# Performance work log

Hardware: AMD Instinct MI355X
Metric: run time of the kernel (lower is better)

Reference implementation:

```python
import jax, jax.numpy as jnp
import numpy as np

T, F, C, V, H, E, S = 256, 32, 8, 10000, 1024, 256, 512
PAD, BOS, EOS = 0, 1, 2


def setup_inputs() -> dict:
    key = jax.random.key(0)
    ks = jax.random.split(key, 16)
    sH = 1.0 / np.sqrt(H).astype(np.float32)
    inp = {
        'token_ctx': jax.random.normal(ks[0], (1, S, H), jnp.float32),
        'char_emb_w': jax.random.normal(ks[1], (V, E), jnp.float32) * 0.02,
        'enc_W_ih': jax.random.normal(ks[2], (3 * H, E), jnp.float32) * sH,
        'enc_W_hh': jax.random.normal(ks[3], (3 * H, H), jnp.float32) * sH,
        'enc_b_ih': jnp.zeros((3 * H,), jnp.float32),
        'enc_b_hh': jnp.zeros((3 * H,), jnp.float32),
        'dec_W_ih': jax.random.normal(ks[4], (3 * H, E), jnp.float32) * sH,
        'dec_W_hh': jax.random.normal(ks[5], (3 * H, H), jnp.float32) * sH,
        'dec_b_ih': jnp.zeros((3 * H,), jnp.float32),
        'dec_b_hh': jnp.zeros((3 * H,), jnp.float32),
        'out_W': jax.random.normal(ks[6], (V, H), jnp.float32) * sH,
        'out_b': jnp.zeros((V,), jnp.float32),
    }
    # (token_id, xtoken_idx, char_id) triples; every token 1..T has exactly C chars
    tok_ids = jnp.repeat(jnp.arange(1, T + 1, dtype=jnp.int32), C)
    xt_ids = jax.random.randint(ks[7], (T * C,), 0, S, jnp.int32)
    ch_ids = jax.random.randint(ks[8], (T * C,), 4, V, jnp.int32)  # avoid specials
    inp['in_sent_token_chars'] = jnp.stack([tok_ids, xt_ids, ch_ids], axis=-1)[None]
    gold = jax.random.randint(ks[9], (T * F,), 4, V, jnp.int32)  # no EOS -> full-length decode
    inp['out_chars'] = jnp.concatenate([jnp.array([BOS], jnp.int32), gold])[None]
    inp['max_tokens'] = T
    inp['max_form_len'] = F
    inp['use_teacher_forcing'] = 1
    return inp


def _gru_cell(x, h, W_ih, W_hh, b_ih, b_hh):
    # PyTorch GRU cell convention; x:[T,E], h:[T,H]
    gi = x @ W_ih.T + b_ih
    gh = h @ W_hh.T + b_hh
    i_r, i_z, i_n = jnp.split(gi, 3, axis=-1)
    h_r, h_z, h_n = jnp.split(gh, 3, axis=-1)
    r = jax.nn.sigmoid(i_r + h_r)
    z = jax.nn.sigmoid(i_z + h_z)
    n = jnp.tanh(i_n + r * h_n)
    return (1.0 - z) * n + z * h


def reference(token_ctx, char_emb_w, enc_W_ih, enc_W_hh, enc_b_ih, enc_b_hh,
              dec_W_ih, dec_W_hh, dec_b_ih, dec_b_hh, out_W, out_b,
              in_sent_token_chars, out_chars, max_tokens, max_form_len,
              use_teacher_forcing):
    Vout = out_b.shape[0]
    # ragged mask select per token id -> here every token has exactly C chars
    tc = in_sent_token_chars[0].reshape(max_tokens, -1, 3)  # [T, C, 3]
    chars = tc[:, :, 2]          # [T, C]
    xtoken_ids = tc[:, :, 1]     # [T, C]
    # enc_state = mean over the token's xtoken contexts
    h0 = jnp.mean(token_ctx[0][xtoken_ids], axis=1)  # [T, H]
    # ---- encoder GRU over the token's chars (batched over tokens) ----
    x_enc = char_emb_w[chars]  # [T, C, E]

    def enc_step(h, x):
        return _gru_cell(x, h, enc_W_ih, enc_W_hh, enc_b_ih, enc_b_hh), None

    h_enc, _ = jax.lax.scan(enc_step, h0, jnp.swapaxes(x_enc, 0, 1))  # [T, H]
    # ---- decoder GRU, max_form_len steps, teacher-forced, EOS freeze+pad ----
    # gold char for token t at step s is out_chars[0, t*F + s + 1]
    gold = out_chars[0, 1:1 + max_tokens * max_form_len].reshape(max_tokens, max_form_len)
    c0 = jnp.full((max_tokens,), out_chars[0, 0], dtype=out_chars.dtype)
    done0 = (c0 == EOS)
    last0 = jnp.zeros((max_tokens, Vout), jnp.float32)

    def dec_step(carry, g):
        h, c, done, last = carry
        x = char_emb_w[c]
        h_new = _gru_cell(x, h, dec_W_ih, dec_W_hh, dec_b_ih, dec_b_hh)
        s_new = h_new @ out_W.T + out_b
        score = jnp.where(done[:, None], last, s_new)  # pad with last score after EOS
        h = jnp.where(done[:, None], h, h_new)         # state frozen after EOS
        if use_teacher_forcing:
            c_next = g
        else:
            c_next = jnp.argmax(s_new, axis=-1).astype(c.dtype)
        done = done | (c_next == EOS)
        return (h, c_next, done, score), score

    _, scores = jax.lax.scan(dec_step, (h_enc, c0, done0, last0),
                             jnp.swapaxes(gold, 0, 1))  # [F, T, V]
    # torch.cat(dec_scores, dim=1): token-major, step-minor -> [1, T*F, V]
    return jnp.transpose(scores, (1, 0, 2)).reshape(1, max_tokens * max_form_len, Vout)
```

## Files before the change

### kernel.cpp

```cpp
#include <hip/hip_runtime.h>
#include <hip/hip_bf16.h>
#include <math.h>

#define TT   256
#define FF   32
#define CCH  8
#define VV   10000
#define HH   1024
#define EE   256
#define NG   3072
#define EOS_ID 2
#define NSTEPS 40
#define CHAIN_BLKS 256
#define CTR_INTS 512

typedef __attribute__((ext_vector_type(8))) short bf16x8;
typedef __attribute__((ext_vector_type(4))) float f32x4;

__device__ __forceinline__ void gload_lds16(const void* g, void* l) {
    __builtin_amdgcn_global_load_lds((const __attribute__((address_space(1))) void*)g,
                                     (__attribute__((address_space(3))) void*)l,
                                     16, 0, 0);
}

__device__ __forceinline__ float sigmf(float x) { return 1.f / (1.f + __expf(-x)); }

__global__ __launch_bounds__(256) void prep_kernel(const int* __restrict__ oc,
                                                   int* __restrict__ c_in,
                                                   unsigned char* __restrict__ done,
                                                   int* __restrict__ ctr) {
    int t = threadIdx.x;
    for (int i = t; i < CTR_INTS; i += 256) ctr[i] = 0;
    int c0 = oc[0];
    bool d = (c0 == EOS_ID);
    for (int f = 0; f < FF; ++f) {
        c_in[t * FF + f] = (f == 0) ? c0 : oc[1 + t * FF + f - 1];
        done[t * FF + f] = d ? 1 : 0;
        d = d || (oc[1 + t * FF + f] == EOS_ID);
    }
}

__global__ __launch_bounds__(256) void h0_kernel(const float* __restrict__ tctx,
                                                 const int* __restrict__ sent,
                                                 float* __restrict__ h,
                                                 __hip_bfloat16* __restrict__ A0) {
    int t = blockIdx.x;
    int tid = threadIdx.x;
    __shared__ int xt[CCH];
    if (tid < CCH) xt[tid] = sent[(t * CCH + tid) * 3 + 1];
    __syncthreads();
#pragma unroll
    for (int jj = 0; jj < 4; ++jj) {
        int j = tid + jj * 256;
        float s = 0.f;
#pragma unroll
        for (int c = 0; c < CCH; ++c) s += tctx[(size_t)xt[c] * HH + j];
        float hv = s * 0.125f;
        h[(size_t)t * HH + j] = hv;
        A0[(size_t)t * HH + j] = __float2bfloat16(hv);
    }
}

__global__ __launch_bounds__(256) void f2b_kernel(const float* __restrict__ src,
                                                  __hip_bfloat16* __restrict__ dst) {
    size_t base = ((size_t)blockIdx.x * 256 + threadIdx.x) * 4;
    float4 v = *(const float4*)(src + base);
    dst[base + 0] = __float2bfloat16(v.x);
    dst[base + 1] = __float2bfloat16(v.y);
    dst[base + 2] = __float2bfloat16(v.z);
    dst[base + 3] = __float2bfloat16(v.w);
}

__global__ __launch_bounds__(256) void build_Bg(const float* __restrict__ Whh,
                                                __hip_bfloat16* __restrict__ Bg) {
    int by = blockIdx.x;
    int tid = threadIdx.x;
    int jbrow = by & 127;
    int jb = by >> 7;
    int g = jbrow >> 5, ji = jbrow & 31;
    __hip_bfloat16* drow = Bg + (size_t)by * HH;
    if (g < 3) {
        const float* srow = Whh + (size_t)(g * 1024 + jb * 32 + ji) * HH;
        float4 v = *(const float4*)(srow + tid * 4);
        drow[tid * 4 + 0] = __float2bfloat16(v.x);
        drow[tid * 4 + 1] = __float2bfloat16(v.y);
        drow[tid * 4 + 2] = __float2bfloat16(v.z);
        drow[tid * 4 + 3] = __float2bfloat16(v.w);
    } else {
        __hip_bfloat16 z = __float2bfloat16(0.f);
        drow[tid * 4 + 0] = z; drow[tid * 4 + 1] = z;
        drow[tid * 4 + 2] = z; drow[tid * 4 + 3] = z;
    }
}

template<int MODE>
__global__ __launch_bounds__(256) void gemm_pipe(const __hip_bfloat16* __restrict__ A, int lda,
                                                 const __hip_bfloat16* __restrict__ B, int ldb,
                                                 float* __restrict__ C,
                                                 const int* __restrict__ idsrc,
                                                 int NIT) {
    __shared__ __hip_bfloat16 As[4][128 * 32];
    __shared__ __hip_bfloat16 Bs[4][128 * 32];
    __shared__ int sids[128];

    const int tid = threadIdx.x;
    const int n0 = blockIdx.x * 128;
    const int m0 = blockIdx.y * 128;

    if (tid < 128) {
        int row = m0 + tid;
        int t = row & 255;
        int id;
        if (MODE == 1) { int c = row >> 8; id = idsrc[(t * CCH + c) * 3 + 2]; }
        else           { int f = row >> 8; id = idsrc[t * FF + f]; }
        sids[tid] = id;
    }
    __syncthreads();

    const int srow = tid >> 2, skq = tid & 3;
    const int l = tid & 63;
    const int w = tid >> 6;
    const int wr = (w >> 1) * 64, wc = (w & 1) * 64;
    const int fra = ((wr + (l & 15)) << 5) + ((l >> 4) << 3);
    const int frb = ((wc + (l & 15)) << 5) + ((l >> 4) << 3);

    f32x4 acc[4][4];
#pragma unroll
    for (int i = 0; i < 4; ++i)
#pragma unroll
        for (int j = 0; j < 4; ++j) acc[i][j] = (f32x4){0.f, 0.f, 0.f, 0.f};

    auto stage = [&](int slot, int it) {
        const int k0 = it * 32;
        const __hip_bfloat16* ga0 = A + (size_t)sids[srow] * lda + k0 + skq * 8;
        const __hip_bfloat16* ga1 = A + (size_t)sids[64 + srow] * lda + k0 + skq * 8;
        const __hip_bfloat16* gb0 = B + (size_t)(n0 + srow) * ldb + k0 + skq * 8;
        const __hip_bfloat16* gb1 = B + (size_t)(n0 + 64 + srow) * ldb + k0 + skq * 8;
        __hip_bfloat16* lA = &As[slot][tid * 8];
        __hip_bfloat16* lB = &Bs[slot][tid * 8];
        gload_lds16(ga0, lA);
        gload_lds16(ga1, lA + 2048);
        gload_lds16(gb0, lB);
        gload_lds16(gb1, lB + 2048);
    };

    stage(0, 0);
    stage(1, 1);

    for (int it = 0; it < NIT; ++it) {
        if (it + 2 < NIT) stage((it + 2) & 3, it + 2);
        int ahead = NIT - 1 - it; if (ahead > 2) ahead = 2;
        if (ahead >= 2)      asm volatile("s_waitcnt vmcnt(8)" ::: "memory");
        else if (ahead == 1) asm volatile("s_waitcnt vmcnt(4)" ::: "memory");
        else                 asm volatile("s_waitcnt vmcnt(0)" ::: "memory");
        __builtin_amdgcn_s_barrier();
        __builtin_amdgcn_sched_barrier(0);

        const __hip_bfloat16* cA = As[it & 3];
        const __hip_bfloat16* cB = Bs[it & 3];
        bf16x8 af[4], bfv[4];
#pragma unroll
        for (int fm = 0; fm < 4; ++fm) af[fm] = *(const bf16x8*)&cA[fra + fm * 512];
#pragma unroll
        for (int fn = 0; fn < 4; ++fn) bfv[fn] = *(const bf16x8*)&cB[frb + fn * 512];
#pragma unroll
        for (int fm = 0; fm < 4; ++fm)
#pragma unroll
            for (int fn = 0; fn < 4; ++fn)
                acc[fm][fn] = __builtin_amdgcn_mfma_f32_16x16x32_bf16(af[fm], bfv[fn], acc[fm][fn], 0, 0, 0);
    }

    const int colb = wc + (l & 15);
    const int rb   = wr + ((l >> 4) << 2);
#pragma unroll
    for (int fm = 0; fm < 4; ++fm)
#pragma unroll
        for (int fn = 0; fn < 4; ++fn)
#pragma unroll
            for (int q = 0; q < 4; ++q)
                C[(size_t)(m0 + rb + fm * 16 + q) * NG + n0 + colb + fn * 16] = acc[fm][fn][q];
}

__global__ __launch_bounds__(256, 1) void chain_kernel(
    __hip_bfloat16* Abuf0, __hip_bfloat16* Abuf1,
    const __hip_bfloat16* __restrict__ Bg_e,
    const __hip_bfloat16* __restrict__ Bg_d,
    const float* __restrict__ gi_enc, const float* __restrict__ gi_dec,
    const float* __restrict__ ebih, const float* __restrict__ ebhh,
    const float* __restrict__ dbih, const float* __restrict__ dbhh,
    const float* __restrict__ hA,
    __hip_bfloat16* __restrict__ hsb,
    const unsigned char* __restrict__ dflags,
    int* flags) {

    __shared__ __align__(16) char smem[52224];

    const int tid = threadIdx.x;
    const int b = blockIdx.x;
    const int mt = b >> 5, jb = b & 31;
    const int m0 = mt * 32;

    const int l = tid & 63, w = tid >> 6;
    const int wr = (w >> 1) * 16;
    const int wc = (w & 1) * 48;
    const int ji = tid & 31;
    const int tr0 = tid >> 5;
    const int j = jb * 32 + ji;

    float* gp = (float*)(smem + 36864);
    __hip_bfloat16* stb = (__hip_bfloat16*)(smem + 36864 + 12800);

    float hreg[4];
#pragma unroll
    for (int p = 0; p < 4; ++p)
        hreg[p] = hA[(size_t)(m0 + p * 8 + tr0) * HH + j];

    const float e_br = ebih[j] + ebhh[j];
    const float e_bz = ebih[HH + j] + ebhh[HH + j];
    const float e_bi = ebih[2 * HH + j];
    const float e_bh = ebhh[2 * HH + j];
    const float d_br = dbih[j] + dbhh[j];
    const float d_bz = dbih[HH + j] + dbhh[HH + j];
    const float d_bi = dbih[2 * HH + j];
    const float d_bh = dbhh[2 * HH + j];

    auto stageB = [&](const __hip_bfloat16* Bp, int slot, int it) {
        char* sb = smem + slot * 12288;
#pragma unroll
        for (int c = 0; c < 3; ++c) {
            int chunk = c * 256 + tid;
            int row = chunk >> 3, q = chunk & 7;
            const __hip_bfloat16* src =
                Bp + (size_t)(jb * 128 + row) * HH + it * 64 + ((q ^ (row & 7)) << 3);
            gload_lds16(src, sb + chunk * 16);
        }
    };

    stageB(Bg_e, 0, 0);
    stageB(Bg_e, 1, 1);

    float gr[4], gz[4], gn_[4];
    int dfl[4] = {0, 0, 0, 0};
#pragma unroll
    for (int p = 0; p < 4; ++p) {
        const float* gb = gi_enc + (size_t)(m0 + p * 8 + tr0) * NG + j;
        asm volatile("global_load_dword %0, %1, off nt" : "=v"(gr[p])  : "v"(gb));
        asm volatile("global_load_dword %0, %1, off nt" : "=v"(gz[p])  : "v"(gb + HH));
        asm volatile("global_load_dword %0, %1, off nt" : "=v"(gn_[p]) : "v"(gb + 2 * HH));
    }

    for (int s = 0; s < NSTEPS; ++s) {
        const __hip_bfloat16* Ab = (s & 1) ? Abuf1 : Abuf0;
        __hip_bfloat16* An = (s & 1) ? Abuf0 : Abuf1;
        const __hip_bfloat16* Bg = (s < CCH) ? Bg_e : Bg_d;

        const __hip_bfloat16* aptr = Ab + (size_t)(m0 + wr + (l & 15)) * HH + ((l >> 4) << 3);
        bf16x8 av[16][2];
#pragma unroll
        for (int it = 0; it < 16; ++it) {
            asm volatile("global_load_dwordx4 %0, %1, off sc0 sc1"
                         : "=v"(av[it][0]) : "v"(aptr + it * 64));
            asm volatile("global_load_dwordx4 %0, %1, off sc0 sc1"
                         : "=v"(av[it][1]) : "v"(aptr + it * 64 + 32));
        }

        f32x4 acc[3];
        acc[0] = (f32x4){0.f, 0.f, 0.f, 0.f};
        acc[1] = (f32x4){0.f, 0.f, 0.f, 0.f};
        acc[2] = (f32x4){0.f, 0.f, 0.f, 0.f};

#pragma unroll
        for (int it = 0; it < 16; ++it) {
            if (it + 2 < 16) stageB(Bg, (it + 2) % 3, it + 2);
            if (it == 0)       asm volatile("s_waitcnt vmcnt(33)" ::: "memory");
            else if (it == 1)  asm volatile("s_waitcnt vmcnt(34)" ::: "memory");
            else if (it <= 13) asm volatile("s_waitcnt vmcnt(6)"  ::: "memory");
            else if (it == 14) asm volatile("s_waitcnt vmcnt(3)"  ::: "memory");
            else               asm volatile("s_waitcnt vmcnt(0)"  ::: "memory");
            __builtin_amdgcn_s_barrier();
            __builtin_amdgcn_sched_barrier(0);

            const __hip_bfloat16* cB = (const __hip_bfloat16*)(smem + (it % 3) * 12288);
#pragma unroll
            for (int kh = 0; kh < 2; ++kh) {
                const int qg = kh * 4 + (l >> 4);
                bf16x8 bf0, bf1, bf2;
                { int r_ = wc + (l & 15);      bf0 = *(const bf16x8*)&cB[r_ * 64 + ((qg ^ (r_ & 7)) << 3)]; }
                { int r_ = wc + 16 + (l & 15); bf1 = *(const bf16x8*)&cB[r_ * 64 + ((qg ^ (r_ & 7)) << 3)]; }
                { int r_ = wc + 32 + (l & 15); bf2 = *(const bf16x8*)&cB[r_ * 64 + ((qg ^ (r_ & 7)) << 3)]; }
                acc[0] = __builtin_amdgcn_mfma_f32_16x16x32_bf16(av[it][kh], bf0, acc[0], 0, 0, 0);
                acc[1] = __builtin_amdgcn_mfma_f32_16x16x32_bf16(av[it][kh], bf1, acc[1], 0, 0, 0);
                acc[2] = __builtin_amdgcn_mfma_f32_16x16x32_bf16(av[it][kh], bf2, acc[2], 0, 0, 0);
            }
        }

        {
            const int rb = wr + ((l >> 4) << 2);
#pragma unroll
            for (int fn = 0; fn < 3; ++fn)
#pragma unroll
                for (int q = 0; q < 4; ++q)
                    gp[(rb + q) * 100 + wc + fn * 16 + (l & 15)] = acc[fn][q];
        }
        __syncthreads();

        const int f = s - CCH;
        const float br_ = (s < CCH) ? e_br : d_br;
        const float bz_ = (s < CCH) ? e_bz : d_bz;
        const float bi_ = (s < CCH) ? e_bi : d_bi;
        const float bh_ = (s < CCH) ? e_bh : d_bh;
#pragma unroll
        for (int p = 0; p < 4; ++p) {
            const int tr = p * 8 + tr0;
            float racc = gp[tr * 100 + ji];
            float zacc = gp[tr * 100 + 32 + ji];
            float nacc = gp[tr * 100 + 64 + ji];
            float r = sigmf(gr[p] + br_ + racc);
            float z = sigmf(gz[p] + bz_ + zacc);
            float n = tanhf(gn_[p] + bi_ + r * (nacc + bh_));
            float hold = hreg[p];
            float hv = (1.f - z) * n + z * hold;
            if (s >= CCH && dfl[p]) hv = hold;
            hreg[p] = hv;
            stb[tr * 32 + ji] = __float2bfloat16(hv);
        }
        __syncthreads();

        if (tid < 128) {
            const int row = tid >> 2, part = tid & 3;
            bf16x8 v = *(const bf16x8*)&stb[row * 32 + part * 8];
            if (s < NSTEPS - 1) {
                const __hip_bfloat16* ap = An + (size_t)(m0 + row) * HH + jb * 32 + part * 8;
                asm volatile("global_store_dwordx4 %0, %1, off sc0 sc1"
                             :: "v"(ap), "v"(v) : "memory");
            }
            if (s >= CCH) {
                bf16x8* hp = (bf16x8*)(hsb + ((size_t)f * TT + m0 + row) * HH + jb * 32 + part * 8);
                __builtin_nontemporal_store(v, hp);
            }
        }

        if (s < NSTEPS - 1) {
            const __hip_bfloat16* BgN = (s + 1 < CCH) ? Bg_e : Bg_d;
            stageB(BgN, 0, 0);
            stageB(BgN, 1, 1);
            asm volatile("s_waitcnt vmcnt(6)" ::: "memory");
            __syncthreads();

            if (tid == 0) {
                int v = s + 1;
                int* fp = flags + (mt << 5) + jb;
                asm volatile("global_store_dword %0, %1, off sc0 sc1"
                             :: "v"(fp), "v"(v) : "memory");
            }

            {
                const float* gnext = (s + 1 < CCH) ? (gi_enc + (size_t)(s + 1) * TT * NG)
                                                   : (gi_dec + (size_t)(s + 1 - CCH) * TT * NG);
#pragma unroll
                for (int p = 0; p < 4; ++p) {
                    const float* gb = gnext + (size_t)(m0 + p * 8 + tr0) * NG + j;
                    asm volatile("global_load_dword %0, %1, off nt" : "=v"(gr[p])  : "v"(gb));
                    asm volatile("global_load_dword %0, %1, off nt" : "=v"(gz[p])  : "v"(gb + HH));
                    asm volatile("global_load_dword %0, %1, off nt" : "=v"(gn_[p]) : "v"(gb + 2 * HH));
                }
                if (s + 1 >= CCH) {
                    const int fnx = s + 1 - CCH;
#pragma unroll
                    for (int p = 0; p < 4; ++p) {
                        const unsigned char* dp = dflags + (size_t)(m0 + p * 8 + tr0) * FF + fnx;
                        asm volatile("global_load_ubyte %0, %1, off" : "=v"(dfl[p]) : "v"(dp));
                    }
                }
            }

            if (tid < 64) {
                const int* fp = flags + (mt << 5) + (tid & 31);
                const int target = s + 1;
                long guard = 0;
                for (;;) {
                    int v = target;
                    if (tid < 32) {
                        asm volatile("global_load_dword %0, %1, off sc0 sc1"
                                     : "=v"(v) : "v"(fp));
                        asm volatile("s_waitcnt vmcnt(0)" ::: "memory");
                    }
                    if (__all(v >= target)) break;
                    if (++guard > (1L << 22)) break;
                    __builtin_amdgcn_s_sleep(4);
                }
            }
            __syncthreads();
        }
    }
}

__global__ __launch_bounds__(256) void scores_pipe(const __hip_bfloat16* __restrict__ hsb,
                                                   const __hip_bfloat16* __restrict__ Wb,
                                                   const float* __restrict__ bout,
                                                   const int* __restrict__ oc,
                                                   float* __restrict__ out) {
    __shared__ __hip_bfloat16 As[4][128 * 32];
    __shared__ __hip_bfloat16 Bs[4][128 * 32];
    int bid = blockIdx.x;
    int sid = (bid & 7) * 632 + (bid >> 3);
    int bx = sid % 79, by = sid / 79;
    int n0 = bx * 128, m0 = by * 128;

    const int tid = threadIdx.x;
    const int l = tid & 63;
    const int w = tid >> 6;
    const int wr = (w >> 1) * 64, wc = (w & 1) * 64;
    const int srow = tid >> 2, skq = tid & 3;

    f32x4 acc[4][4];
#pragma unroll
    for (int i = 0; i < 4; ++i)
#pragma unroll
        for (int j = 0; j < 4; ++j) acc[i][j] = (f32x4){0.f, 0.f, 0.f, 0.f};

    int br0 = n0 + srow, br1 = n0 + 64 + srow;
    br0 = (br0 > VV - 1) ? VV - 1 : br0;
    br1 = (br1 > VV - 1) ? VV - 1 : br1;
    const __hip_bfloat16* gA0 = hsb + (size_t)(m0 + srow) * HH + skq * 8;
    const __hip_bfloat16* gA1 = hsb + (size_t)(m0 + 64 + srow) * HH + skq * 8;
    const __hip_bfloat16* gB0 = Wb + (size_t)br0 * HH + skq * 8;
    const __hip_bfloat16* gB1 = Wb + (size_t)br1 * HH + skq * 8;
    const int fra = ((wr + (l & 15)) << 5) + ((l >> 4) << 3);
    const int frb = ((wc + (l & 15)) << 5) + ((l >> 4) << 3);

    auto stage = [&](int slot, int it) {
        const int k0 = it * 32;
        __hip_bfloat16* lA = &As[slot][tid * 8];
        __hip_bfloat16* lB = &Bs[slot][tid * 8];
        gload_lds16(gA0 + k0, lA);
        gload_lds16(gA1 + k0, lA + 2048);
        gload_lds16(gB0 + k0, lB);
        gload_lds16(gB1 + k0, lB + 2048);
    };

    stage(0, 0);
    stage(1, 1);

    for (int it = 0; it < 32; ++it) {
        if (it + 2 < 32) stage((it + 2) & 3, it + 2);
        int ahead = 31 - it; if (ahead > 2) ahead = 2;
        if (ahead >= 2)      asm volatile("s_waitcnt vmcnt(8)" ::: "memory");
        else if (ahead == 1) asm volatile("s_waitcnt vmcnt(4)" ::: "memory");
        else                 asm volatile("s_waitcnt vmcnt(0)" ::: "memory");
        __builtin_amdgcn_s_barrier();
        __builtin_amdgcn_sched_barrier(0);

        const __hip_bfloat16* cA = As[it & 3];
        const __hip_bfloat16* cB = Bs[it & 3];
        bf16x8 af[4], bfv[4];
#pragma unroll
        for (int fm = 0; fm < 4; ++fm) af[fm] = *(const bf16x8*)&cA[fra + fm * 512];
#pragma unroll
        for (int fn = 0; fn < 4; ++fn) bfv[fn] = *(const bf16x8*)&cB[frb + fn * 512];
#pragma unroll
        for (int fm = 0; fm < 4; ++fm)
#pragma unroll
            for (int fn = 0; fn < 4; ++fn)
                acc[fm][fn] = __builtin_amdgcn_mfma_f32_16x16x32_bf16(af[fm], bfv[fn], acc[fm][fn], 0, 0, 0);
    }

    const bool zf = (oc[0] == EOS_ID);
    const int colb = wc + (l & 15);
    const int rb   = wr + ((l >> 4) << 2);
#pragma unroll
    for (int fn = 0; fn < 4; ++fn) {
        int v = n0 + colb + fn * 16;
        if (v < VV) {
            float bb = bout[v];
#pragma unroll
            for (int fm = 0; fm < 4; ++fm) {
#pragma unroll
                for (int q = 0; q < 4; ++q) {
                    int m = m0 + rb + fm * 16 + q;
                    int fo = m >> 8, t = m & 255;
                    float val = zf ? 0.f : (acc[fm][fn][q] + bb);
                    __builtin_nontemporal_store(val, &out[(size_t)(t * FF + fo) * VV + v]);
                }
            }
        }
    }
}

extern "C" void kernel_launch(void* const* d_in, const int* in_sizes, int n_in,
                              void* d_out, int out_size, void* d_ws, size_t ws_size,
                              hipStream_t stream) {
    (void)in_sizes; (void)n_in; (void)ws_size;

    const float* token_ctx = (const float*)d_in[0];
    const float* emb       = (const float*)d_in[1];
    const float* eWih      = (const float*)d_in[2];
    const float* eWhh      = (const float*)d_in[3];
    const float* ebih      = (const float*)d_in[4];
    const float* ebhh      = (const float*)d_in[5];
    const float* dWih      = (const float*)d_in[6];
    const float* dWhh      = (const float*)d_in[7];
    const float* dbih      = (const float*)d_in[8];
    const float* dbhh      = (const float*)d_in[9];
    const float* Wout      = (const float*)d_in[10];
    const float* bout      = (const float*)d_in[11];
    const int*   sent      = (const int*)d_in[12];
    const int*   ochars    = (const int*)d_in[13];
    float* out = (float*)d_out;

    char* w = (char*)d_ws;
    float* hA = (float*)w;                      w += (size_t)TT * HH * 4;
    __hip_bfloat16* Ab0 = (__hip_bfloat16*)w;   w += (size_t)TT * HH * 2;
    __hip_bfloat16* Ab1 = (__hip_bfloat16*)w;   w += (size_t)TT * HH * 2;
    __hip_bfloat16* hsb = (__hip_bfloat16*)w;   w += (size_t)FF * TT * HH * 2;
    __hip_bfloat16* Woutb = (__hip_bfloat16*)w; w += (size_t)VV * HH * 2;
    int* c_in = (int*)w;                        w += (size_t)TT * FF * 4;
    unsigned char* done = (unsigned char*)w;    w += (size_t)TT * FF;
    w = (char*)(((size_t)w + 255) & ~(size_t)255);
    int* ctr = (int*)w;                         w += (size_t)CTR_INTS * 4;

    char* tail = (char*)d_out + (size_t)out_size * 4;
    tail -= (size_t)32 * 128 * HH * 2;    __hip_bfloat16* Bg_e = (__hip_bfloat16*)tail;
    tail -= (size_t)32 * 128 * HH * 2;    __hip_bfloat16* Bg_d = (__hip_bfloat16*)tail;
    tail -= (size_t)CCH * TT * NG * 4;    float* gi_enc = (float*)tail;
    tail -= (size_t)FF * TT * NG * 4;     float* gi_dec = (float*)tail;
    tail -= (size_t)VV * EE * 2;          __hip_bfloat16* emb_bf = (__hip_bfloat16*)tail;
    tail -= (size_t)NG * EE * 2;          __hip_bfloat16* Wihb_e = (__hip_bfloat16*)tail;
    tail -= (size_t)NG * EE * 2;          __hip_bfloat16* Wihb_d = (__hip_bfloat16*)tail;

    prep_kernel<<<1, 256, 0, stream>>>(ochars, c_in, done, ctr);
    h0_kernel<<<TT, 256, 0, stream>>>(token_ctx, sent, hA, Ab0);
    f2b_kernel<<<(VV * EE) / 4 / 256, 256, 0, stream>>>(emb, emb_bf);
    f2b_kernel<<<(NG * EE) / 4 / 256, 256, 0, stream>>>(eWih, Wihb_e);
    f2b_kernel<<<(NG * EE) / 4 / 256, 256, 0, stream>>>(dWih, Wihb_d);
    f2b_kernel<<<(VV * HH) / 4 / 256, 256, 0, stream>>>(Wout, Woutb);
    build_Bg<<<4096, 256, 0, stream>>>(eWhh, Bg_e);
    build_Bg<<<4096, 256, 0, stream>>>(dWhh, Bg_d);

    gemm_pipe<1><<<dim3(24, 16), 256, 0, stream>>>(emb_bf, EE, Wihb_e, EE, gi_enc, sent, 8);
    gemm_pipe<2><<<dim3(24, 64), 256, 0, stream>>>(emb_bf, EE, Wihb_d, EE, gi_dec, c_in, 8);

    chain_kernel<<<CHAIN_BLKS, 256, 0, stream>>>(Ab0, Ab1, Bg_e, Bg_d,
                                                 gi_enc, gi_dec,
                                                 ebih, ebhh, dbih, dbhh,
                                                 hA, hsb, done, ctr);

    scores_pipe<<<5056, 256, 0, stream>>>(hsb, Woutb, bout, ochars, out);
}
```

Measured before the change: 734.9 us.

## Keep recurrent weight slice resident in LDS across chain steps

The persistent GRU chain kernel is retiled so each of 256 blocks owns 64 rows by 16 hidden units (48 gate rows), which lets its whole W_hh slice (96 KB bf16) sit in LDS. The slice is loaded once for the encoder and once for the decoder, instead of streaming B tiles from global memory every step. The padded fourth gate group in the Bg layout is dropped, and the inter-block flag wait moves to the top of each step, polling 64 producer blocks. In exchange the kernel uses about 113 KB of dynamic LDS, each block has more peer blocks to wait on, and the A-operand global loads are now fully serialized with the flag wait.

```diff
diff --git a/kernel.cpp b/kernel.cpp
--- a/kernel.cpp
+++ b/kernel.cpp
@@ -13,6 +13,11 @@
 #define NSTEPS 40
 #define CHAIN_BLKS 256
 #define CTR_INTS 512
+
+#define LDS_B_BYTES   98304
+#define LDS_GP_OFF    98304
+#define LDS_STB_OFF   (98304 + 13312)
+#define LDS_TOTAL     (98304 + 13312 + 2048)
 
 typedef __attribute__((ext_vector_type(8))) short bf16x8;
 typedef __attribute__((ext_vector_type(4))) float f32x4;
@@ -71,26 +76,19 @@
     dst[base + 3] = __float2bfloat16(v.w);
 }
 
-__global__ __launch_bounds__(256) void build_Bg(const float* __restrict__ Whh,
-                                                __hip_bfloat16* __restrict__ Bg) {
+__global__ __launch_bounds__(256) void build_Bg2(const float* __restrict__ Whh,
+                                                 __hip_bfloat16* __restrict__ Bg) {
     int by = blockIdx.x;
     int tid = threadIdx.x;
-    int jbrow = by & 127;
-    int jb = by >> 7;
-    int g = jbrow >> 5, ji = jbrow & 31;
+    int jb = by / 48, rr = by % 48;
+    int g = rr >> 4, jj = rr & 15;
+    const float* srow = Whh + (size_t)(g * 1024 + jb * 16 + jj) * HH;
     __hip_bfloat16* drow = Bg + (size_t)by * HH;
-    if (g < 3) {
-        const float* srow = Whh + (size_t)(g * 1024 + jb * 32 + ji) * HH;
-        float4 v = *(const float4*)(srow + tid * 4);
-        drow[tid * 4 + 0] = __float2bfloat16(v.x);
-        drow[tid * 4 + 1] = __float2bfloat16(v.y);
-        drow[tid * 4 + 2] = __float2bfloat16(v.z);
-        drow[tid * 4 + 3] = __float2bfloat16(v.w);
-    } else {
-        __hip_bfloat16 z = __float2bfloat16(0.f);
-        drow[tid * 4 + 0] = z; drow[tid * 4 + 1] = z;
-        drow[tid * 4 + 2] = z; drow[tid * 4 + 3] = z;
-    }
+    float4 v = *(const float4*)(srow + tid * 4);
+    drow[tid * 4 + 0] = __float2bfloat16(v.x);
+    drow[tid * 4 + 1] = __float2bfloat16(v.y);
+    drow[tid * 4 + 2] = __float2bfloat16(v.z);
+    drow[tid * 4 + 3] = __float2bfloat16(v.w);
 }
 
 template<int MODE>
@@ -193,27 +191,26 @@
     const unsigned char* __restrict__ dflags,
     int* flags) {
 
-    __shared__ __align__(16) char smem[52224];
+    extern __shared__ __align__(16) char smem[];
+    char* Bs = smem;
+    float* gp = (float*)(smem + LDS_GP_OFF);
+    __hip_bfloat16* stb = (__hip_bfloat16*)(smem + LDS_STB_OFF);
 
     const int tid = threadIdx.x;
     const int b = blockIdx.x;
-    const int mt = b >> 5, jb = b & 31;
-    const int m0 = mt * 32;
+    const int mt = b >> 6, jb = b & 63;
+    const int m0 = mt * 64;
+    const int jbase = jb * 16;
 
     const int l = tid & 63, w = tid >> 6;
-    const int wr = (w >> 1) * 16;
-    const int wc = (w & 1) * 48;
-    const int ji = tid & 31;
-    const int tr0 = tid >> 5;
-    const int j = jb * 32 + ji;
-
-    float* gp = (float*)(smem + 36864);
-    __hip_bfloat16* stb = (__hip_bfloat16*)(smem + 36864 + 12800);
+    const int ji = tid & 15;
+    const int rg = tid >> 4;
+    const int j = jbase + ji;
 
     float hreg[4];
 #pragma unroll
     for (int p = 0; p < 4; ++p)
-        hreg[p] = hA[(size_t)(m0 + p * 8 + tr0) * HH + j];
+        hreg[p] = hA[(size_t)(m0 + p * 16 + rg) * HH + j];
 
     const float e_br = ebih[j] + ebhh[j];
     const float e_bz = ebih[HH + j] + ebhh[HH + j];
@@ -224,83 +221,95 @@
     const float d_bi = dbih[2 * HH + j];
     const float d_bh = dbhh[2 * HH + j];
 
-    auto stageB = [&](const __hip_bfloat16* Bp, int slot, int it) {
-        char* sb = smem + slot * 12288;
-#pragma unroll
-        for (int c = 0; c < 3; ++c) {
+    auto stageBfull = [&](const __hip_bfloat16* Bp) {
+#pragma unroll
+        for (int c = 0; c < 24; ++c) {
             int chunk = c * 256 + tid;
-            int row = chunk >> 3, q = chunk & 7;
-            const __hip_bfloat16* src =
-                Bp + (size_t)(jb * 128 + row) * HH + it * 64 + ((q ^ (row & 7)) << 3);
-            gload_lds16(src, sb + chunk * 16);
+            int row = chunk >> 7, q = chunk & 127;
+            const char* src = (const char*)(Bp + (size_t)row * HH) + ((q ^ (row & 7)) << 4);
+            gload_lds16(src, Bs + chunk * 16);
         }
     };
 
-    stageB(Bg_e, 0, 0);
-    stageB(Bg_e, 1, 1);
+    auto ldB = [&](int nt, int ks) -> bf16x8 {
+        int r = nt * 16 + (l & 15);
+        int g = ks * 4 + (l >> 4);
+        return *(const bf16x8*)(Bs + r * 2048 + ((g ^ (r & 7)) << 4));
+    };
 
     float gr[4], gz[4], gn_[4];
     int dfl[4] = {0, 0, 0, 0};
 #pragma unroll
     for (int p = 0; p < 4; ++p) {
-        const float* gb = gi_enc + (size_t)(m0 + p * 8 + tr0) * NG + j;
+        const float* gb = gi_enc + (size_t)(m0 + p * 16 + rg) * NG + j;
         asm volatile("global_load_dword %0, %1, off nt" : "=v"(gr[p])  : "v"(gb));
         asm volatile("global_load_dword %0, %1, off nt" : "=v"(gz[p])  : "v"(gb + HH));
         asm volatile("global_load_dword %0, %1, off nt" : "=v"(gn_[p]) : "v"(gb + 2 * HH));
     }
 
     for (int s = 0; s < NSTEPS; ++s) {
+        if (s > 0) {
+            if (tid < 64) {
+                const int* fp = flags + (mt << 6) + l;
+                long guard = 0;
+                for (;;) {
+                    int v;
+                    asm volatile("global_load_dword %0, %1, off sc0 sc1" : "=v"(v) : "v"(fp));
+                    asm volatile("s_waitcnt vmcnt(0)" ::: "memory");
+                    if (__all(v >= s)) break;
+                    if (++guard > (1L << 22)) break;
+                    __builtin_amdgcn_s_sleep(2);
+                }
+            }
+            __syncthreads();
+        }
+
+        if (s == 0 || s == CCH) {
+            stageBfull(((s == 0) ? Bg_e : Bg_d) + (size_t)jb * 48 * HH);
+            asm volatile("s_waitcnt vmcnt(0)" ::: "memory");
+            __syncthreads();
+        }
+
         const __hip_bfloat16* Ab = (s & 1) ? Abuf1 : Abuf0;
         __hip_bfloat16* An = (s & 1) ? Abuf0 : Abuf1;
-        const __hip_bfloat16* Bg = (s < CCH) ? Bg_e : Bg_d;
-
-        const __hip_bfloat16* aptr = Ab + (size_t)(m0 + wr + (l & 15)) * HH + ((l >> 4) << 3);
-        bf16x8 av[16][2];
-#pragma unroll
-        for (int it = 0; it < 16; ++it) {
+
+        asm volatile("s_waitcnt vmcnt(0)" ::: "memory");
+        const __hip_bfloat16* aptr = Ab + (size_t)(m0 + w * 16 + (l & 15)) * HH + ((l >> 4) << 3);
+        bf16x8 av[32];
+#pragma unroll
+        for (int ks = 0; ks < 32; ++ks)
             asm volatile("global_load_dwordx4 %0, %1, off sc0 sc1"
-                         : "=v"(av[it][0]) : "v"(aptr + it * 64));
-            asm volatile("global_load_dwordx4 %0, %1, off sc0 sc1"
-                         : "=v"(av[it][1]) : "v"(aptr + it * 64 + 32));
-        }
+                         : "=v"(av[ks]) : "v"(aptr + ks * 32));
 
         f32x4 acc[3];
         acc[0] = (f32x4){0.f, 0.f, 0.f, 0.f};
         acc[1] = (f32x4){0.f, 0.f, 0.f, 0.f};
         acc[2] = (f32x4){0.f, 0.f, 0.f, 0.f};
 
-#pragma unroll
-        for (int it = 0; it < 16; ++it) {
-            if (it + 2 < 16) stageB(Bg, (it + 2) % 3, it + 2);
-            if (it == 0)       asm volatile("s_waitcnt vmcnt(33)" ::: "memory");
-            else if (it == 1)  asm volatile("s_waitcnt vmcnt(34)" ::: "memory");
-            else if (it <= 13) asm volatile("s_waitcnt vmcnt(6)"  ::: "memory");
-            else if (it == 14) asm volatile("s_waitcnt vmcnt(3)"  ::: "memory");
-            else               asm volatile("s_waitcnt vmcnt(0)"  ::: "memory");
-            __builtin_amdgcn_s_barrier();
+        bf16x8 bb[3][3];
+#pragma unroll
+        for (int nt = 0; nt < 3; ++nt) { bb[0][nt] = ldB(nt, 0); bb[1][nt] = ldB(nt, 1); }
+
+#pragma unroll
+        for (int ks = 0; ks < 32; ++ks) {
+            if (ks + 2 < 32) {
+#pragma unroll
+                for (int nt = 0; nt < 3; ++nt) bb[(ks + 2) % 3][nt] = ldB(nt, ks + 2);
+            }
+            asm volatile("s_waitcnt vmcnt(%0)" :: "i"(31 - ks) : "memory");
             __builtin_amdgcn_sched_barrier(0);
-
-            const __hip_bfloat16* cB = (const __hip_bfloat16*)(smem + (it % 3) * 12288);
-#pragma unroll
-            for (int kh = 0; kh < 2; ++kh) {
-                const int qg = kh * 4 + (l >> 4);
-                bf16x8 bf0, bf1, bf2;
-                { int r_ = wc + (l & 15);      bf0 = *(const bf16x8*)&cB[r_ * 64 + ((qg ^ (r_ & 7)) << 3)]; }
-                { int r_ = wc + 16 + (l & 15); bf1 = *(const bf16x8*)&cB[r_ * 64 + ((qg ^ (r_ & 7)) << 3)]; }
-                { int r_ = wc + 32 + (l & 15); bf2 = *(const bf16x8*)&cB[r_ * 64 + ((qg ^ (r_ & 7)) << 3)]; }
-                acc[0] = __builtin_amdgcn_mfma_f32_16x16x32_bf16(av[it][kh], bf0, acc[0], 0, 0, 0);
-                acc[1] = __builtin_amdgcn_mfma_f32_16x16x32_bf16(av[it][kh], bf1, acc[1], 0, 0, 0);
-                acc[2] = __builtin_amdgcn_mfma_f32_16x16x32_bf16(av[it][kh], bf2, acc[2], 0, 0, 0);
-            }
+            acc[0] = __builtin_amdgcn_mfma_f32_16x16x32_bf16(av[ks], bb[ks % 3][0], acc[0], 0, 0, 0);
+            acc[1] = __builtin_amdgcn_mfma_f32_16x16x32_bf16(av[ks], bb[ks % 3][1], acc[1], 0, 0, 0);
+            acc[2] = __builtin_amdgcn_mfma_f32_16x16x32_bf16(av[ks], bb[ks % 3][2], acc[2], 0, 0, 0);
         }
 
         {
-            const int rb = wr + ((l >> 4) << 2);
-#pragma unroll
-            for (int fn = 0; fn < 3; ++fn)
+            const int rb = w * 16 + ((l >> 4) << 2);
+#pragma unroll
+            for (int nt = 0; nt < 3; ++nt)
 #pragma unroll
                 for (int q = 0; q < 4; ++q)
-                    gp[(rb + q) * 100 + wc + fn * 16 + (l & 15)] = acc[fn][q];
+                    gp[(rb + q) * 52 + nt * 16 + (l & 15)] = acc[nt][q];
         }
         __syncthreads();
 
@@ -311,10 +320,10 @@
         const float bh_ = (s < CCH) ? e_bh : d_bh;
 #pragma unroll
         for (int p = 0; p < 4; ++p) {
-            const int tr = p * 8 + tr0;
-            float racc = gp[tr * 100 + ji];
-            float zacc = gp[tr * 100 + 32 + ji];
-            float nacc = gp[tr * 100 + 64 + ji];
+            const int tr = p * 16 + rg;
+            float racc = gp[tr * 52 + ji];
+            float zacc = gp[tr * 52 + 16 + ji];
+            float nacc = gp[tr * 52 + 32 + ji];
             float r = sigmf(gr[p] + br_ + racc);
             float z = sigmf(gz[p] + bz_ + zacc);
             float n = tanhf(gn_[p] + bi_ + r * (nacc + bh_));
@@ -322,44 +331,39 @@
             float hv = (1.f - z) * n + z * hold;
             if (s >= CCH && dfl[p]) hv = hold;
             hreg[p] = hv;
-            stb[tr * 32 + ji] = __float2bfloat16(hv);
+            stb[tr * 16 + ji] = __float2bfloat16(hv);
         }
         __syncthreads();
 
         if (tid < 128) {
-            const int row = tid >> 2, part = tid & 3;
-            bf16x8 v = *(const bf16x8*)&stb[row * 32 + part * 8];
+            const int row = tid >> 1, part = tid & 1;
+            bf16x8 v = *(const bf16x8*)&stb[row * 16 + part * 8];
             if (s < NSTEPS - 1) {
-                const __hip_bfloat16* ap = An + (size_t)(m0 + row) * HH + jb * 32 + part * 8;
+                const __hip_bfloat16* ap = An + (size_t)(m0 + row) * HH + jbase + part * 8;
                 asm volatile("global_store_dwordx4 %0, %1, off sc0 sc1"
                              :: "v"(ap), "v"(v) : "memory");
             }
             if (s >= CCH) {
-                bf16x8* hp = (bf16x8*)(hsb + ((size_t)f * TT + m0 + row) * HH + jb * 32 + part * 8);
+                bf16x8* hp = (bf16x8*)(hsb + ((size_t)f * TT + m0 + row) * HH + jbase + part * 8);
                 __builtin_nontemporal_store(v, hp);
             }
         }
 
         if (s < NSTEPS - 1) {
-            const __hip_bfloat16* BgN = (s + 1 < CCH) ? Bg_e : Bg_d;
-            stageB(BgN, 0, 0);
-            stageB(BgN, 1, 1);
-            asm volatile("s_waitcnt vmcnt(6)" ::: "memory");
+            asm volatile("s_waitcnt vmcnt(0)" ::: "memory");
             __syncthreads();
-
             if (tid == 0) {
                 int v = s + 1;
-                int* fp = flags + (mt << 5) + jb;
+                int* fp = flags + (mt << 6) + jb;
                 asm volatile("global_store_dword %0, %1, off sc0 sc1"
                              :: "v"(fp), "v"(v) : "memory");
             }
-
             {
                 const float* gnext = (s + 1 < CCH) ? (gi_enc + (size_t)(s + 1) * TT * NG)
                                                    : (gi_dec + (size_t)(s + 1 - CCH) * TT * NG);
 #pragma unroll
                 for (int p = 0; p < 4; ++p) {
-                    const float* gb = gnext + (size_t)(m0 + p * 8 + tr0) * NG + j;
+                    const float* gb = gnext + (size_t)(m0 + p * 16 + rg) * NG + j;
                     asm volatile("global_load_dword %0, %1, off nt" : "=v"(gr[p])  : "v"(gb));
                     asm volatile("global_load_dword %0, %1, off nt" : "=v"(gz[p])  : "v"(gb + HH));
                     asm volatile("global_load_dword %0, %1, off nt" : "=v"(gn_[p]) : "v"(gb + 2 * HH));
@@ -368,29 +372,11 @@
                     const int fnx = s + 1 - CCH;
 #pragma unroll
                     for (int p = 0; p < 4; ++p) {
-                        const unsigned char* dp = dflags + (size_t)(m0 + p * 8 + tr0) * FF + fnx;
+                        const unsigned char* dp = dflags + (size_t)(m0 + p * 16 + rg) * FF + fnx;
                         asm volatile("global_load_ubyte %0, %1, off" : "=v"(dfl[p]) : "v"(dp));
                     }
                 }
             }
-
-            if (tid < 64) {
-                const int* fp = flags + (mt << 5) + (tid & 31);
-                const int target = s + 1;
-                long guard = 0;
-                for (;;) {
-                    int v = target;
-                    if (tid < 32) {
-                        asm volatile("global_load_dword %0, %1, off sc0 sc1"
-                                     : "=v"(v) : "v"(fp));
-                        asm volatile("s_waitcnt vmcnt(0)" ::: "memory");
-                    }
-                    if (__all(v >= target)) break;
-                    if (++guard > (1L << 22)) break;
-                    __builtin_amdgcn_s_sleep(4);
-                }
-            }
-            __syncthreads();
         }
     }
 }
@@ -520,13 +506,16 @@
     int* ctr = (int*)w;                         w += (size_t)CTR_INTS * 4;
 
     char* tail = (char*)d_out + (size_t)out_size * 4;
-    tail -= (size_t)32 * 128 * HH * 2;    __hip_bfloat16* Bg_e = (__hip_bfloat16*)tail;
-    tail -= (size_t)32 * 128 * HH * 2;    __hip_bfloat16* Bg_d = (__hip_bfloat16*)tail;
+    tail -= (size_t)NG * HH * 2;          __hip_bfloat16* Bg_e = (__hip_bfloat16*)tail;
+    tail -= (size_t)NG * HH * 2;          __hip_bfloat16* Bg_d = (__hip_bfloat16*)tail;
     tail -= (size_t)CCH * TT * NG * 4;    float* gi_enc = (float*)tail;
     tail -= (size_t)FF * TT * NG * 4;     float* gi_dec = (float*)tail;
     tail -= (size_t)VV * EE * 2;          __hip_bfloat16* emb_bf = (__hip_bfloat16*)tail;
     tail -= (size_t)NG * EE * 2;          __hip_bfloat16* Wihb_e = (__hip_bfloat16*)tail;
     tail -= (size_t)NG * EE * 2;          __hip_bfloat16* Wihb_d = (__hip_bfloat16*)tail;
+
+    hipFuncSetAttribute((const void*)chain_kernel,
+                        hipFuncAttributeMaxDynamicSharedMemorySize, LDS_TOTAL);
 
     prep_kernel<<<1, 256, 0, stream>>>(ochars, c_in, done, ctr);
     h0_kernel<<<TT, 256, 0, stream>>>(token_ctx, sent, hA, Ab0);
@@ -534,16 +523,16 @@
     f2b_kernel<<<(NG * EE) / 4 / 256, 256, 0, stream>>>(eWih, Wihb_e);
     f2b_kernel<<<(NG * EE) / 4 / 256, 256, 0, stream>>>(dWih, Wihb_d);
     f2b_kernel<<<(VV * HH) / 4 / 256, 256, 0, stream>>>(Wout, Woutb);
-    build_Bg<<<4096, 256, 0, stream>>>(eWhh, Bg_e);
-    build_Bg<<<4096, 256, 0, stream>>>(dWhh, Bg_d);
+    build_Bg2<<<NG, 256, 0, stream>>>(eWhh, Bg_e);
+    build_Bg2<<<NG, 256, 0, stream>>>(dWhh, Bg_d);
 
     gemm_pipe<1><<<dim3(24, 16), 256, 0, stream>>>(emb_bf, EE, Wihb_e, EE, gi_enc, sent, 8);
     gemm_pipe<2><<<dim3(24, 64), 256, 0, stream>>>(emb_bf, EE, Wihb_d, EE, gi_dec, c_in, 8);
 
-    chain_kernel<<<CHAIN_BLKS, 256, 0, stream>>>(Ab0, Ab1, Bg_e, Bg_d,
-                                                 gi_enc, gi_dec,
-                                                 ebih, ebhh, dbih, dbhh,
-                                                 hA, hsb, done, ctr);
+    chain_kernel<<<CHAIN_BLKS, 256, LDS_TOTAL, stream>>>(Ab0, Ab1, Bg_e, Bg_d,
+                                                         gi_enc, gi_dec,
+                                                         ebih, ebhh, dbih, dbhh,
+                                                         hA, hsb, done, ctr);
 
     scores_pipe<<<5056, 256, 0, stream>>>(hsb, Woutb, bout, ochars, out);
 }
```

After: 697.9 us. -5.0%, faster.
